# Kernel tuning notes

Measured on AMD Instinct MI355X. Metric: run time of the kernel, lower is better.

Reference implementation:

```python
import jax, jax.numpy as jnp
import numpy as np

BETA = 0.05

def _mogrify(x, h, Qd, Rd):
    x = 2.0 * jax.nn.sigmoid(h @ Qd) * x
    h = 2.0 * jax.nn.sigmoid(x @ Rd) * h
    x = 2.0 * jax.nn.sigmoid(h @ Qd) * x
    h = 2.0 * jax.nn.sigmoid(x @ Rd) * h
    return x, h

def _gru_cell(x, h, Wih, Whh, bih, bhh):
    gi = x @ Wih.T + bih
    gh = h @ Whh.T + bhh
    i_r, i_z, i_n = jnp.split(gi, 3, axis=-1)
    h_r, h_z, h_n = jnp.split(gh, 3, axis=-1)
    r = jax.nn.sigmoid(i_r + h_r)
    z = jax.nn.sigmoid(i_z + h_z)
    n = jnp.tanh(i_n + r * h_n)
    return (1.0 - z) * n + z * h

def _scan_dir(xT, mT, Qd, Rd, Wih, Whh, bih, bhh):
    # xT: [T,B,D], mT: [T,B] bool. Masked GRU scan == packed-sequence semantics.
    B = xT.shape[1]
    H = Whh.shape[1]
    def step(h, inp):
        xt, m = inp
        xm, hm = _mogrify(xt, h, Qd, Rd)
        hn = _gru_cell(xm, hm, Wih, Whh, bih, bhh)
        h = jnp.where(m[:, None], hn, h)
        out = jnp.where(m[:, None], hn, 0.0)
        return h, out
    h0 = jnp.zeros((B, H), xT.dtype)
    _, out = jax.lax.scan(step, h0, (xT, mT))
    return out  # [T,B,H]

def setup_inputs() -> dict:
    key = jax.random.key(0)
    ks = jax.random.split(key, 16)
    B, T, D, H, V, E, S, L = 64, 1024, 256, 256, 50000, 8, 256, 19
    rng = np.random.RandomState(0)
    lens = np.sort(rng.randint(T // 2, T + 1, size=B))[::-1].copy()
    lens[0] = T
    entity_masks = rng.randint(0, 2, size=(B, E)); entity_masks[:, 0] = 1
    slice_masks = rng.randint(0, 2, size=(B, S)); slice_masks[:, 0] = 1
    slice_lens = slice_masks.sum(axis=1).astype(np.float32)
    sc = 1.0 / np.sqrt(H).astype(np.float32)
    inp = {
        'sents': jax.random.randint(ks[0], (B, T), 0, V, dtype=jnp.int32),
        'lens': jnp.asarray(lens, dtype=jnp.int32),
        'entities': jax.random.randint(ks[1], (B, E), 0, T // 2, dtype=jnp.int32),
        'slices': jax.random.randint(ks[2], (B, S), 0, T // 2, dtype=jnp.int32),
        'slice_lens': jnp.asarray(slice_lens),
        'entity_masks': jnp.asarray(entity_masks, dtype=jnp.int32),
        'slice_masks': jnp.asarray(slice_masks, dtype=jnp.int32),
        'emb_table': jax.random.normal(ks[3], (V, D), jnp.float32) * 0.1,
        'Q': jax.random.normal(ks[4], (2, H, D), jnp.float32) * sc,
        'R': jax.random.normal(ks[5], (2, D, H), jnp.float32) * sc,
        'Wih_f': jax.random.normal(ks[6], (3 * H, D), jnp.float32) * sc,
        'Whh_f': jax.random.normal(ks[7], (3 * H, H), jnp.float32) * sc,
        'bih_f': jnp.zeros((3 * H,), jnp.float32),
        'bhh_f': jnp.zeros((3 * H,), jnp.float32),
        'Wih_b': jax.random.normal(ks[8], (3 * H, D), jnp.float32) * sc,
        'Whh_b': jax.random.normal(ks[9], (3 * H, H), jnp.float32) * sc,
        'bih_b': jnp.zeros((3 * H,), jnp.float32),
        'bhh_b': jnp.zeros((3 * H,), jnp.float32),
        'ent_W': jax.random.normal(ks[10], (1, H), jnp.float32) * sc,
        'ent_b': jnp.zeros((1,), jnp.float32),
        'att_w': jax.random.normal(ks[11], (1, H, 1), jnp.float32),
        'dense_W': jax.random.normal(ks[12], (L, H), jnp.float32) * sc,
        'dense_b': jnp.zeros((L,), jnp.float32),
    }
    return inp

def reference(sents, lens, entities, slices, slice_lens, entity_masks, slice_masks,
              emb_table, Q, R, Wih_f, Whh_f, bih_f, bhh_f, Wih_b, Whh_b, bih_b, bhh_b,
              ent_W, ent_b, att_w, dense_W, dense_b):
    B, T = sents.shape
    H = Whh_f.shape[1]
    x = emb_table[sents]                                   # [B,T,D] (dropout = eval identity)
    mask = jnp.arange(T)[None, :] < lens[:, None]          # [B,T]
    xT = jnp.transpose(x, (1, 0, 2))
    mT = mask.T
    out_f = _scan_dir(xT, mT, Q[0], R[0], Wih_f, Whh_f, bih_f, bhh_f)
    out_b = _scan_dir(xT[::-1], mT[::-1], Q[1], R[1], Wih_b, Whh_b, bih_b, bhh_b)[::-1]
    enc = jnp.transpose(out_f + out_b, (1, 0, 2))          # [B,T,H]

    E = entities.shape[1]; S = slices.shape[1]
    ee = jnp.take_along_axis(enc, jnp.broadcast_to(entities[:, :, None].astype(jnp.int32), (B, E, H)), axis=1)
    es = jnp.take_along_axis(enc, jnp.broadcast_to(slices[:, :, None].astype(jnp.int32), (B, S, H)), axis=1)

    # gate_attention
    ew = jnp.squeeze(ee @ ent_W.T + ent_b, axis=-1)        # [B,E]
    ew = jnp.where(entity_masks == 0, -jnp.inf, ew)
    ew = jax.nn.softmax(ew, axis=-1)
    entity = jnp.einsum('be,beh->bh', ew, ee)
    p = jnp.tanh(entity)                                   # [B,H]
    words = jnp.einsum('bsh,bh->bs', es, p)
    words = jnp.where(slice_masks == 0, -jnp.inf, words)
    ww = jax.nn.softmax(words, axis=-1) * slice_lens[:, None]
    rela = jnp.where(ww > BETA, ww, 0.0) / slice_lens[:, None]
    rela = rela / jnp.max(rela, axis=1, keepdims=True)
    Hcat = jnp.concatenate([ee, rela[:, :, None] * es], axis=1)  # [B,E+S,H]

    # attention
    M = jnp.tanh(Hcat)
    a = jnp.einsum('bnh,h->bn', M, att_w[0, :, 0])
    a = jnp.where(a == 0, -jnp.inf, a)
    score = jax.nn.softmax(a, axis=-1)
    att = jnp.einsum('bn,bnh->bh', score, Hcat)
    return jnp.tanh(att) @ dense_W.T + dense_b             # [B,19]
```

## Files before the change

### kernel.cpp

```cpp
#include <hip/hip_runtime.h>
#include <hip/hip_fp16.h>
#include <math.h>

typedef unsigned int uint;

#define Bsz 64
#define Tt  1024
#define TH  512

#define HMF   1280
#define PARTF 1792
#define SMEMF 14080

typedef _Float16 h2 __attribute__((ext_vector_type(2)));
#if defined(__has_builtin)
#if __has_builtin(__builtin_amdgcn_fdot2)
#define HAS_FDOT2 1
#endif
#endif

__device__ __forceinline__ float sigm(float x){ return 1.f/(1.f+expf(-x)); }

#define LG0  asm volatile("s_waitcnt lgkmcnt(0)":::"memory")
#define BAR  __builtin_amdgcn_s_barrier

__device__ __forceinline__ void dot2b(uint w, uint a0, uint a1, float& s0, float& s1){
  h2 wh = __builtin_bit_cast(h2, w);
#ifdef HAS_FDOT2
  s0 = __builtin_amdgcn_fdot2(wh, __builtin_bit_cast(h2,a0), s0, false);
  s1 = __builtin_amdgcn_fdot2(wh, __builtin_bit_cast(h2,a1), s1, false);
#else
  h2 x0 = __builtin_bit_cast(h2,a0), x1 = __builtin_bit_cast(h2,a1);
  s0 = fmaf((float)wh.x,(float)x0.x, fmaf((float)wh.y,(float)x0.y, s0));
  s1 = fmaf((float)wh.x,(float)x1.x, fmaf((float)wh.y,(float)x1.y, s1));
#endif
}

__global__ void pack_k(const float* __restrict__ Q, const float* __restrict__ R,
                       const float* __restrict__ Wih_f, const float* __restrict__ Whh_f,
                       const float* __restrict__ Wih_b, const float* __restrict__ Whh_b,
                       __half* __restrict__ Wh)
{
  int ci = blockIdx.x*256 + threadIdx.x;
  if (ci >= 131072) return;
  float v[8];
  if (ci < 32768){
    bool isR = ci >= 16384;
    int c0 = ci & 16383;
    int c = c0 & 255;
    int rest = c0 >> 8;
    int u = rest & 3, dw = rest >> 2;
    int w = dw & 7, d = dw >> 3;
    const float* S = (isR ? R : Q) + d*65536;
    int k0 = 32*w + 8*u;
    #pragma unroll
    for (int j=0;j<8;++j) v[j] = S[(k0+j)*256 + c];
  } else {
    int c0 = ci - 32768;
    int c = c0 & 255;
    int rest = c0 >> 8;
    int e = rest % 24, dw = rest / 24;
    int w = dw & 7, d = dw >> 3;
    int mat = w & 1, ks = w >> 1;
    int u8 = e / 3, g = e % 3;
    const float* W = mat ? (d? Whh_b : Whh_f) : (d? Wih_b : Wih_f);
    const float* row = W + (size_t)(g*256 + c)*256 + (64*ks + 8*u8);
    #pragma unroll
    for (int j=0;j<8;++j) v[j] = row[j];
  }
  __half h8[8];
  #pragma unroll
  for (int j=0;j<8;++j) h8[j] = __float2half(v[j]);
  *(uint4*)(Wh + (size_t)ci*8) = *(uint4*)h8;
}

__global__ __launch_bounds__(512, 1) void scan_k(
    const int* __restrict__ sents, const int* __restrict__ lens,
    const float* __restrict__ emb,
    const float* __restrict__ bih_f, const float* __restrict__ bhh_f,
    const float* __restrict__ bih_b, const float* __restrict__ bhh_b,
    const __half* __restrict__ Wh, float* __restrict__ enc)
{
  extern __shared__ float sm[];
  __half* smH = (__half*)sm;

  const int bx = blockIdx.x;
  const int dir  = ((bx & 7) >= 4) ? 1 : 0;
  const int pair = (bx >> 3)*4 + (bx & 3);
  const int b0 = pair*2;
  const int tid = threadIdx.x;
  const int wv = tid >> 6, ln = tid & 63;
  const int cj = tid & 255, cb = tid >> 8;
  const int matE = wv & 1, ksE = wv >> 1;

  const __half* QB = Wh + (size_t)((dir*8+wv)*4)*2048;
  const __half* RB = Wh + 131072 + (size_t)((dir*8+wv)*4)*2048;
  const __half* Gp = Wh + 262144 + (size_t)((dir*8+wv)*24)*2048;
  const float* bih = dir ? bih_b : bih_f;
  const float* bhh = dir ? bhh_b : bhh_f;

  const int len0 = lens[b0], len1 = lens[b0+1];
  const int mylen = cb ? len1 : len0;
  const float bi_r = bih[cj], bi_z = bih[cj+256], bi_n = bih[cj+512];
  const float bh_r = bhh[cj], bh_z = bhh[cj+256], bh_n = bhh[cj+512];

  int nsteps, t, tstep;
  if (!dir){ nsteps = TH; t = 0; tstep = 1; }
  else { int mx = max(len0,len1); nsteps = mx; t = mx-1; tstep = -1; }

  smH[512 + tid] = (__half)0.f;

  uint4 Qr[16], Rr[16];
  {
    const uint4* q4 = (const uint4*)QB;
    const uint4* r4 = (const uint4*)RB;
    #pragma unroll
    for (int u=0; u<4; ++u)
      #pragma unroll
      for (int q=0; q<4; ++q){
        Qr[u*4+q] = q4[u*256 + q*64 + ln];
        Rr[u*4+q] = r4[u*256 + q*64 + ln];
      }
  }

  auto dot4 = [&](const uint4& W, const uint4& A0, const uint4& A1, float& a0, float& a1){
    dot2b(W.x, A0.x, A1.x, a0, a1);
    dot2b(W.y, A0.y, A1.y, a0, a1);
    dot2b(W.z, A0.z, A1.z, a0, a1);
    dot2b(W.w, A0.w, A1.w, a0, a1);
  };

  auto mog_part = [&](int actsHO, const uint4 (&W)[16]){
    float2 acc[4];
    acc[0]=acc[1]=acc[2]=acc[3]=make_float2(0.f,0.f);
    #pragma unroll
    for (int u=0; u<4; ++u){
      const int k8 = 4*wv + u;
      const uint4 a0 = *(const uint4*)(smH + actsHO + k8*8);
      const uint4 a1 = *(const uint4*)(smH + actsHO + 256 + k8*8);
      dot4(W[u*4+0], a0, a1, acc[0].x, acc[0].y);
      dot4(W[u*4+1], a0, a1, acc[1].x, acc[1].y);
      dot4(W[u*4+2], a0, a1, acc[2].x, acc[2].y);
      dot4(W[u*4+3], a0, a1, acc[3].x, acc[3].y);
    }
    #pragma unroll
    for (int q=0;q<4;++q)
      *(float2*)(sm + PARTF + wv*512 + (ln+64*q)*2) = acc[q];
  };
  auto mog_fin = [&](float mult, int dstHO, bool alsoF32)->float{
    float ssum = 0.f;
    #pragma unroll
    for (int p=0;p<8;++p) ssum += sm[PARTF + p*512 + cj*2 + cb];
    float val = 2.f*sigm(ssum)*mult;
    smH[dstHO + cb*256 + cj] = (__half)val;
    if (alsoF32) sm[HMF + cb*256 + cj] = val;
    return val;
  };

  uint4 GA[4], GBb[4], GC[4];
  #define LDU(DST, U) do{ const uint4* p_ = (const uint4*)(Gp + (size_t)(U)*2048); \
    DST[0]=p_[ln]; DST[1]=p_[ln+64]; DST[2]=p_[ln+128]; DST[3]=p_[ln+192]; }while(0)
  LDU(GA, 0); LDU(GBb, 1);

  float hprev = 0.f, x1 = 0.f, hm1 = 0.f;
  LG0; BAR();

  for (int s=0; s<nsteps; ++s, t+=tstep){
    int tok = sents[(b0+cb)*Tt + t];
    float x0 = emb[(size_t)tok*256 + cj];

    mog_part(512, Qr);              LG0; BAR();
    x1 = mog_fin(x0, 0, false);     LG0; BAR();
    mog_part(0, Rr);                LG0; BAR();
    hm1 = mog_fin(hprev, 1024, false); LG0; BAR();
    mog_part(1024, Qr);             LG0; BAR();
    x1 = mog_fin(x1, 0, false);     LG0; BAR();
    mog_part(0, Rr);                LG0; BAR();
    mog_fin(hm1, 1024, true);       LG0; BAR();

    {
      const int AFh = matE ? 1024 : 0;
      float2 ag[12];
      #pragma unroll
      for (int i=0;i<12;++i) ag[i] = make_float2(0.f,0.f);

      #define E_STEP(E, CUR, NXT, NU) { \
        LDU(NXT, NU); \
        const int u8_ = (E)/3, g_ = (E) - 3*u8_; \
        const int kb_ = 64*ksE + 8*u8_; \
        const uint4 ea0 = *(const uint4*)(smH + AFh + kb_); \
        const uint4 ea1 = *(const uint4*)(smH + AFh + 256 + kb_); \
        dot4(CUR[0], ea0, ea1, ag[g_*4+0].x, ag[g_*4+0].y); \
        dot4(CUR[1], ea0, ea1, ag[g_*4+1].x, ag[g_*4+1].y); \
        dot4(CUR[2], ea0, ea1, ag[g_*4+2].x, ag[g_*4+2].y); \
        dot4(CUR[3], ea0, ea1, ag[g_*4+3].x, ag[g_*4+3].y); }

      E_STEP(0,  GA,  GC,  2);  E_STEP(1,  GBb, GA,  3);  E_STEP(2,  GC,  GBb, 4);
      E_STEP(3,  GA,  GC,  5);  E_STEP(4,  GBb, GA,  6);  E_STEP(5,  GC,  GBb, 7);
      E_STEP(6,  GA,  GC,  8);  E_STEP(7,  GBb, GA,  9);  E_STEP(8,  GC,  GBb, 10);
      E_STEP(9,  GA,  GC,  11); E_STEP(10, GBb, GA,  12); E_STEP(11, GC,  GBb, 13);
      E_STEP(12, GA,  GC,  14); E_STEP(13, GBb, GA,  15); E_STEP(14, GC,  GBb, 16);
      E_STEP(15, GA,  GC,  17); E_STEP(16, GBb, GA,  18); E_STEP(17, GC,  GBb, 19);
      E_STEP(18, GA,  GC,  20); E_STEP(19, GBb, GA,  21); E_STEP(20, GC,  GBb, 22);
      E_STEP(21, GA,  GC,  23); E_STEP(22, GBb, GA,  0);  E_STEP(23, GC,  GBb, 1);
      #undef E_STEP

      #pragma unroll
      for (int g=0;g<3;++g)
        #pragma unroll
        for (int q=0;q<4;++q)
          *(float2*)(sm + PARTF + wv*1536 + (g*256 + ln + 64*q)*2) = ag[g*4+q];
    }
    LG0; BAR();
    {
      float gi[3], gh[3];
      #pragma unroll
      for (int g=0; g<3; ++g){
        float si = 0.f, sh = 0.f;
        #pragma unroll
        for (int p=0;p<4;++p){
          si += sm[PARTF + (p*2+0)*1536 + (g*256+cj)*2 + cb];
          sh += sm[PARTF + (p*2+1)*1536 + (g*256+cj)*2 + cb];
        }
        gi[g] = si; gh[g] = sh;
      }
      float r = sigm(gi[0]+bi_r + gh[0]+bh_r);
      float z = sigm(gi[1]+bi_z + gh[1]+bh_z);
      float n = tanhf(gi[2]+bi_n + r*(gh[2]+bh_n));
      float hm2v = sm[HMF + cb*256 + cj];
      float uu = (1.f - z)*n + z*hm2v;
      bool m = (t < mylen);
      float hnew = m ? uu : hprev;
      hprev = hnew;
      smH[512 + cb*256 + cj] = (__half)hnew;
      if (m && t < TH)
        atomicAdd(&enc[((size_t)(b0+cb)*TH + t)*256 + cj], uu);
    }
    LG0; BAR();
  }
  #undef LDU
}

__global__ __launch_bounds__(256) void epi_k(
    const float* __restrict__ enc,
    const int* __restrict__ entities, const int* __restrict__ slices,
    const float* __restrict__ slice_lens,
    const int* __restrict__ entity_masks, const int* __restrict__ slice_masks,
    const float* __restrict__ ent_W, const float* __restrict__ ent_b,
    const float* __restrict__ att_w,
    const float* __restrict__ dense_W, const float* __restrict__ dense_b,
    float* __restrict__ out)
{
    const int b = blockIdx.x;
    const int j = threadIdx.x;
    const int wave = j >> 6, lane = j & 63;

    __shared__ float ee[8][256];
    __shared__ float p[256];
    __shared__ float rela[256];
    __shared__ float sc[264];
    __shared__ float red[4];
    __shared__ float aw[256];
    __shared__ int   spos[256];

    aw[j]   = att_w[j];
    spos[j] = slices[b * 256 + j];
    #pragma unroll
    for (int e = 0; e < 8; ++e)
        ee[e][j] = enc[((size_t)b * TH + entities[b * 8 + e]) * 256 + j];
    __syncthreads();

    float entWj = ent_W[j];
    for (int e = 0; e < 8; ++e) {
        float v = ee[e][j] * entWj;
        #pragma unroll
        for (int o = 32; o > 0; o >>= 1) v += __shfl_down(v, o);
        if (lane == 0) red[wave] = v;
        __syncthreads();
        if (j == 0) sc[e] = red[0] + red[1] + red[2] + red[3] + ent_b[0];
        __syncthreads();
    }
    float mx = -INFINITY;
    float ewv[8];
    #pragma unroll
    for (int e = 0; e < 8; ++e) {
        float v = entity_masks[b * 8 + e] ? sc[e] : -INFINITY;
        ewv[e] = v; mx = fmaxf(mx, v);
    }
    float den = 0.f;
    #pragma unroll
    for (int e = 0; e < 8; ++e) {
        ewv[e] = entity_masks[b * 8 + e] ? expf(ewv[e] - mx) : 0.f;
        den += ewv[e];
    }
    float accp = 0.f;
    #pragma unroll
    for (int e = 0; e < 8; ++e) accp += (ewv[e] / den) * ee[e][j];
    p[j] = tanhf(accp);
    __syncthreads();

    for (int s0 = wave; s0 < 256; s0 += 4) {
        const float* row = enc + ((size_t)b * TH + spos[s0]) * 256;
        float v = 0.f;
        #pragma unroll
        for (int i = 0; i < 4; ++i) { int c = lane + 64 * i; v += row[c] * p[c]; }
        #pragma unroll
        for (int o = 32; o > 0; o >>= 1) v += __shfl_down(v, o);
        if (lane == 0) sc[s0] = v;
    }
    __syncthreads();

    float sl  = slice_lens[b];
    int   smk = slice_masks[b * 256 + j];
    float wv  = smk ? sc[j] : -INFINITY;
    float bm = wv;
    #pragma unroll
    for (int o = 32; o > 0; o >>= 1) bm = fmaxf(bm, __shfl_down(bm, o));
    __syncthreads();
    if (lane == 0) red[wave] = bm;
    __syncthreads();
    bm = fmaxf(fmaxf(red[0], red[1]), fmaxf(red[2], red[3]));
    float ex = smk ? expf(wv - bm) : 0.f;
    float sm2 = ex;
    #pragma unroll
    for (int o = 32; o > 0; o >>= 1) sm2 += __shfl_down(sm2, o);
    __syncthreads();
    if (lane == 0) red[wave] = sm2;
    __syncthreads();
    sm2 = red[0] + red[1] + red[2] + red[3];
    float ww = ex / sm2 * sl;
    float rl = (ww > 0.05f) ? (ww / sl) : 0.f;
    float rm = rl;
    #pragma unroll
    for (int o = 32; o > 0; o >>= 1) rm = fmaxf(rm, __shfl_down(rm, o));
    __syncthreads();
    if (lane == 0) red[wave] = rm;
    __syncthreads();
    rm = fmaxf(fmaxf(red[0], red[1]), fmaxf(red[2], red[3]));
    rl = rl / rm;
    rela[j] = rl;
    __syncthreads();

    for (int n = wave; n < 264; n += 4) {
        float v = 0.f;
        if (n < 8) {
            #pragma unroll
            for (int i = 0; i < 4; ++i) { int c = lane + 64 * i; v += tanhf(ee[n][c]) * aw[c]; }
        } else {
            int s0 = n - 8;
            const float* row = enc + ((size_t)b * TH + spos[s0]) * 256;
            float rl2 = rela[s0];
            #pragma unroll
            for (int i = 0; i < 4; ++i) { int c = lane + 64 * i; v += tanhf(rl2 * row[c]) * aw[c]; }
        }
        #pragma unroll
        for (int o = 32; o > 0; o >>= 1) v += __shfl_down(v, o);
        if (lane == 0) sc[n] = v;
    }
    __syncthreads();

    float a1 = sc[j];       a1 = (a1 == 0.f) ? -INFINITY : a1;
    float a2 = (j < 8) ? sc[256 + j] : -INFINITY;
    if (a2 == 0.f) a2 = -INFINITY;
    float am = fmaxf(a1, a2);
    #pragma unroll
    for (int o = 32; o > 0; o >>= 1) am = fmaxf(am, __shfl_down(am, o));
    __syncthreads();
    if (lane == 0) red[wave] = am;
    __syncthreads();
    am = fmaxf(fmaxf(red[0], red[1]), fmaxf(red[2], red[3]));
    float e1 = (a1 == -INFINITY) ? 0.f : expf(a1 - am);
    float e2 = (a2 == -INFINITY) ? 0.f : expf(a2 - am);
    float esum = e1 + e2;
    #pragma unroll
    for (int o = 32; o > 0; o >>= 1) esum += __shfl_down(esum, o);
    __syncthreads();
    if (lane == 0) red[wave] = esum;
    __syncthreads();
    esum = red[0] + red[1] + red[2] + red[3];
    __syncthreads();
    sc[j] = e1 / esum;
    if (j < 8) sc[256 + j] = e2 / esum;
    __syncthreads();

    float att = 0.f;
    #pragma unroll
    for (int n = 0; n < 8; ++n) att += sc[n] * ee[n][j];
    for (int s0 = 0; s0 < 256; ++s0) {
        float scn = sc[8 + s0];
        if (scn > 0.f)
            att += scn * rela[s0] * enc[((size_t)b * TH + spos[s0]) * 256 + j];
    }
    float ta = tanhf(att);

    for (int l = 0; l < 19; ++l) {
        float v = ta * dense_W[l * 256 + j];
        #pragma unroll
        for (int o = 32; o > 0; o >>= 1) v += __shfl_down(v, o);
        __syncthreads();
        if (lane == 0) red[wave] = v;
        __syncthreads();
        if (j == 0) out[b * 19 + l] = red[0] + red[1] + red[2] + red[3] + dense_b[l];
    }
}

extern "C" void kernel_launch(void* const* d_in, const int* in_sizes, int n_in,
                              void* d_out, int out_size, void* d_ws, size_t ws_size,
                              hipStream_t stream) {
    (void)in_sizes; (void)n_in; (void)out_size; (void)ws_size;
    const int*   sents        = (const int*)d_in[0];
    const int*   lens         = (const int*)d_in[1];
    const int*   entities     = (const int*)d_in[2];
    const int*   slices       = (const int*)d_in[3];
    const float* slice_lens   = (const float*)d_in[4];
    const int*   entity_masks = (const int*)d_in[5];
    const int*   slice_masks  = (const int*)d_in[6];
    const float* emb          = (const float*)d_in[7];
    const float* Q            = (const float*)d_in[8];
    const float* R            = (const float*)d_in[9];
    const float* Wih_f        = (const float*)d_in[10];
    const float* Whh_f        = (const float*)d_in[11];
    const float* bih_f        = (const float*)d_in[12];
    const float* bhh_f        = (const float*)d_in[13];
    const float* Wih_b        = (const float*)d_in[14];
    const float* Whh_b        = (const float*)d_in[15];
    const float* bih_b        = (const float*)d_in[16];
    const float* bhh_b        = (const float*)d_in[17];
    const float* ent_W        = (const float*)d_in[18];
    const float* ent_b        = (const float*)d_in[19];
    const float* att_w        = (const float*)d_in[20];
    const float* dense_W      = (const float*)d_in[21];
    const float* dense_b      = (const float*)d_in[22];

    float*  enc = (float*)d_ws;
    __half* Wh  = (__half*)(enc + (size_t)Bsz * TH * 256);

    const int smem_bytes = SMEMF * 4;
    hipFuncSetAttribute(reinterpret_cast<const void*>(scan_k),
                        hipFuncAttributeMaxDynamicSharedMemorySize, smem_bytes);

    hipMemsetAsync(enc, 0, (size_t)Bsz * TH * 256 * sizeof(float), stream);
    pack_k<<<512, 256, 0, stream>>>(Q, R, Wih_f, Whh_f, Wih_b, Whh_b, Wh);
    scan_k<<<64, 512, smem_bytes, stream>>>(sents, lens, emb,
                                            bih_f, bhh_f, bih_b, bhh_b,
                                            Wh, enc);
    epi_k<<<64, 256, 0, stream>>>(enc, entities, slices, slice_lens,
                                  entity_masks, slice_masks, ent_W, ent_b,
                                  att_w, dense_W, dense_b, (float*)d_out);
}
```

Baseline: 11.10 ms.

## Double scan block to 1024 threads and stream mogrifier weights from cache

Each scan block grows from 512 to 1024 threads (16 waves), so every wave handles half as much of the K dimension in the mogrifier and GRU gate matvecs. The Q/R mogrifier weights are no longer held in registers; they are reloaded from global/L2 each sub-step, with a small prefetch of the next matrix slice. Partial sums come from twice as many waves, so shared memory grows and the reductions read more slices, while only the first 512 threads run the elementwise finish steps. The aim is more latency hiding per serial timestep, at the cost of repeated weight traffic, extra reduction work and idle threads during the finish phases.

```diff
diff --git a/kernel.cpp b/kernel.cpp
--- a/kernel.cpp
+++ b/kernel.cpp
@@ -10,7 +10,7 @@
 
 #define HMF   1280
 #define PARTF 1792
-#define SMEMF 14080
+#define SMEMF 26368
 
 typedef _Float16 h2 __attribute__((ext_vector_type(2)));
 #if defined(__has_builtin)
@@ -74,7 +74,7 @@
   *(uint4*)(Wh + (size_t)ci*8) = *(uint4*)h8;
 }
 
-__global__ __launch_bounds__(512, 1) void scan_k(
+__global__ __launch_bounds__(1024) void scan_k(
     const int* __restrict__ sents, const int* __restrict__ lens,
     const float* __restrict__ emb,
     const float* __restrict__ bih_f, const float* __restrict__ bhh_f,
@@ -90,12 +90,19 @@
   const int b0 = pair*2;
   const int tid = threadIdx.x;
   const int wv = tid >> 6, ln = tid & 63;
-  const int cj = tid & 255, cb = tid >> 8;
-  const int matE = wv & 1, ksE = wv >> 1;
-
-  const __half* QB = Wh + (size_t)((dir*8+wv)*4)*2048;
-  const __half* RB = Wh + 131072 + (size_t)((dir*8+wv)*4)*2048;
-  const __half* Gp = Wh + 262144 + (size_t)((dir*8+wv)*24)*2048;
+  const int cj = tid & 255;
+  const int cb = (tid >> 8) & 1;
+  const bool fin = (tid < 512);
+  const int matE = wv & 1, ks8 = wv >> 1;
+
+  const uint4* QB2 = (const uint4*)Wh
+      + (size_t)(((dir*8 + (wv>>1))*4 + (wv&1)*2))*256;
+  const uint4* RB2 = (const uint4*)(Wh + 131072)
+      + (size_t)(((dir*8 + (wv>>1))*4 + (wv&1)*2))*256;
+  const int wold = matE + 2*(ks8>>1);
+  const uint4* Gp4 = (const uint4*)(Wh + 262144)
+      + ((size_t)(dir*8 + wold)*24 + 12*(ks8&1))*256;
+
   const float* bih = dir ? bih_b : bih_f;
   const float* bhh = dir ? bhh_b : bhh_f;
 
@@ -108,20 +115,7 @@
   if (!dir){ nsteps = TH; t = 0; tstep = 1; }
   else { int mx = max(len0,len1); nsteps = mx; t = mx-1; tstep = -1; }
 
-  smH[512 + tid] = (__half)0.f;
-
-  uint4 Qr[16], Rr[16];
-  {
-    const uint4* q4 = (const uint4*)QB;
-    const uint4* r4 = (const uint4*)RB;
-    #pragma unroll
-    for (int u=0; u<4; ++u)
-      #pragma unroll
-      for (int q=0; q<4; ++q){
-        Qr[u*4+q] = q4[u*256 + q*64 + ln];
-        Rr[u*4+q] = r4[u*256 + q*64 + ln];
-      }
-  }
+  if (tid < 512) smH[512 + tid] = (__half)0.f;
 
   auto dot4 = [&](const uint4& W, const uint4& A0, const uint4& A1, float& a0, float& a1){
     dot2b(W.x, A0.x, A1.x, a0, a1);
@@ -130,18 +124,33 @@
     dot2b(W.w, A0.w, A1.w, a0, a1);
   };
 
-  auto mog_part = [&](int actsHO, const uint4 (&W)[16]){
+  uint4 P0, P1, P2, P3;
+  { P0 = QB2[ln]; P1 = QB2[ln+64]; P2 = QB2[ln+128]; P3 = QB2[ln+192]; }
+
+  auto mog_part = [&](int actsHO, const uint4* ub, const uint4* nextb){
+    uint4 W00=P0, W01=P1, W02=P2, W03=P3;
+    uint4 W10 = ub[256+ln], W11 = ub[256+ln+64],
+          W12 = ub[256+ln+128], W13 = ub[256+ln+192];
+    P0 = nextb[ln]; P1 = nextb[ln+64]; P2 = nextb[ln+128]; P3 = nextb[ln+192];
     float2 acc[4];
     acc[0]=acc[1]=acc[2]=acc[3]=make_float2(0.f,0.f);
-    #pragma unroll
-    for (int u=0; u<4; ++u){
-      const int k8 = 4*wv + u;
+    {
+      const int k8 = 2*wv;
       const uint4 a0 = *(const uint4*)(smH + actsHO + k8*8);
       const uint4 a1 = *(const uint4*)(smH + actsHO + 256 + k8*8);
-      dot4(W[u*4+0], a0, a1, acc[0].x, acc[0].y);
-      dot4(W[u*4+1], a0, a1, acc[1].x, acc[1].y);
-      dot4(W[u*4+2], a0, a1, acc[2].x, acc[2].y);
-      dot4(W[u*4+3], a0, a1, acc[3].x, acc[3].y);
+      dot4(W00, a0, a1, acc[0].x, acc[0].y);
+      dot4(W01, a0, a1, acc[1].x, acc[1].y);
+      dot4(W02, a0, a1, acc[2].x, acc[2].y);
+      dot4(W03, a0, a1, acc[3].x, acc[3].y);
+    }
+    {
+      const int k8 = 2*wv + 1;
+      const uint4 a0 = *(const uint4*)(smH + actsHO + k8*8);
+      const uint4 a1 = *(const uint4*)(smH + actsHO + 256 + k8*8);
+      dot4(W10, a0, a1, acc[0].x, acc[0].y);
+      dot4(W11, a0, a1, acc[1].x, acc[1].y);
+      dot4(W12, a0, a1, acc[2].x, acc[2].y);
+      dot4(W13, a0, a1, acc[3].x, acc[3].y);
     }
     #pragma unroll
     for (int q=0;q<4;++q)
@@ -150,7 +159,7 @@
   auto mog_fin = [&](float mult, int dstHO, bool alsoF32)->float{
     float ssum = 0.f;
     #pragma unroll
-    for (int p=0;p<8;++p) ssum += sm[PARTF + p*512 + cj*2 + cb];
+    for (int p=0;p<16;++p) ssum += sm[PARTF + p*512 + cj*2 + cb];
     float val = 2.f*sigm(ssum)*mult;
     smH[dstHO + cb*256 + cj] = (__half)val;
     if (alsoF32) sm[HMF + cb*256 + cj] = val;
@@ -158,36 +167,44 @@
   };
 
   uint4 GA[4], GBb[4], GC[4];
-  #define LDU(DST, U) do{ const uint4* p_ = (const uint4*)(Gp + (size_t)(U)*2048); \
+  #define LDU(DST, U) do{ const uint4* p_ = Gp4 + (size_t)(U)*256; \
     DST[0]=p_[ln]; DST[1]=p_[ln+64]; DST[2]=p_[ln+128]; DST[3]=p_[ln+192]; }while(0)
-  LDU(GA, 0); LDU(GBb, 1);
 
   float hprev = 0.f, x1 = 0.f, hm1 = 0.f;
   LG0; BAR();
 
   for (int s=0; s<nsteps; ++s, t+=tstep){
-    int tok = sents[(b0+cb)*Tt + t];
-    float x0 = emb[(size_t)tok*256 + cj];
-
-    mog_part(512, Qr);              LG0; BAR();
-    x1 = mog_fin(x0, 0, false);     LG0; BAR();
-    mog_part(0, Rr);                LG0; BAR();
-    hm1 = mog_fin(hprev, 1024, false); LG0; BAR();
-    mog_part(1024, Qr);             LG0; BAR();
-    x1 = mog_fin(x1, 0, false);     LG0; BAR();
-    mog_part(0, Rr);                LG0; BAR();
-    mog_fin(hm1, 1024, true);       LG0; BAR();
+    float x0 = 0.f;
+    if (fin){
+      int tok = sents[(b0+cb)*Tt + t];
+      x0 = emb[(size_t)tok*256 + cj];
+    }
+    mog_part(512, QB2, RB2);        LG0; BAR();
+    if (fin) x1 = mog_fin(x0, 0, false);
+    LG0; BAR();
+    mog_part(0, RB2, QB2);          LG0; BAR();
+    if (fin) hm1 = mog_fin(hprev, 1024, false);
+    LG0; BAR();
+    mog_part(1024, QB2, RB2);       LG0; BAR();
+    if (fin) x1 = mog_fin(x1, 0, false);
+    LG0; BAR();
+    mog_part(0, RB2, QB2);
+    LDU(GA, 0); LDU(GBb, 1);
+    LG0; BAR();
+    if (fin) mog_fin(hm1, 1024, true);
+    LG0; BAR();
 
     {
-      const int AFh = matE ? 1024 : 0;
       float2 ag[12];
       #pragma unroll
       for (int i=0;i<12;++i) ag[i] = make_float2(0.f,0.f);
-
-      #define E_STEP(E, CUR, NXT, NU) { \
-        LDU(NXT, NU); \
-        const int u8_ = (E)/3, g_ = (E) - 3*u8_; \
-        const int kb_ = 64*ksE + 8*u8_; \
+      const int AFh = matE ? 1024 : 0;
+      const int kbb = 32*ks8;
+
+      #define E_STEP(E, CUR, NXT, DOLOAD) { \
+        if (DOLOAD) LDU(NXT, (E)+2); \
+        const int g_ = (E) % 3; \
+        const int kb_ = kbb + 8*((E)/3); \
         const uint4 ea0 = *(const uint4*)(smH + AFh + kb_); \
         const uint4 ea1 = *(const uint4*)(smH + AFh + 256 + kb_); \
         dot4(CUR[0], ea0, ea1, ag[g_*4+0].x, ag[g_*4+0].y); \
@@ -195,32 +212,28 @@
         dot4(CUR[2], ea0, ea1, ag[g_*4+2].x, ag[g_*4+2].y); \
         dot4(CUR[3], ea0, ea1, ag[g_*4+3].x, ag[g_*4+3].y); }
 
-      E_STEP(0,  GA,  GC,  2);  E_STEP(1,  GBb, GA,  3);  E_STEP(2,  GC,  GBb, 4);
-      E_STEP(3,  GA,  GC,  5);  E_STEP(4,  GBb, GA,  6);  E_STEP(5,  GC,  GBb, 7);
-      E_STEP(6,  GA,  GC,  8);  E_STEP(7,  GBb, GA,  9);  E_STEP(8,  GC,  GBb, 10);
-      E_STEP(9,  GA,  GC,  11); E_STEP(10, GBb, GA,  12); E_STEP(11, GC,  GBb, 13);
-      E_STEP(12, GA,  GC,  14); E_STEP(13, GBb, GA,  15); E_STEP(14, GC,  GBb, 16);
-      E_STEP(15, GA,  GC,  17); E_STEP(16, GBb, GA,  18); E_STEP(17, GC,  GBb, 19);
-      E_STEP(18, GA,  GC,  20); E_STEP(19, GBb, GA,  21); E_STEP(20, GC,  GBb, 22);
-      E_STEP(21, GA,  GC,  23); E_STEP(22, GBb, GA,  0);  E_STEP(23, GC,  GBb, 1);
+      E_STEP(0,  GA,  GC,  1); E_STEP(1,  GBb, GA,  1); E_STEP(2,  GC,  GBb, 1);
+      E_STEP(3,  GA,  GC,  1); E_STEP(4,  GBb, GA,  1); E_STEP(5,  GC,  GBb, 1);
+      E_STEP(6,  GA,  GC,  1); E_STEP(7,  GBb, GA,  1); E_STEP(8,  GC,  GBb, 1);
+      E_STEP(9,  GA,  GC,  1); E_STEP(10, GBb, GA,  0); E_STEP(11, GC,  GBb, 0);
       #undef E_STEP
 
       #pragma unroll
       for (int g=0;g<3;++g)
         #pragma unroll
         for (int q=0;q<4;++q)
-          *(float2*)(sm + PARTF + wv*1536 + (g*256 + ln + 64*q)*2) = ag[g*4+q];
-    }
-    LG0; BAR();
-    {
+          *(float2*)(sm + PARTF + (ks8*2+matE)*1536 + (g*256 + ln + 64*q)*2) = ag[g*4+q];
+    }
+    LG0; BAR();
+    if (fin){
       float gi[3], gh[3];
       #pragma unroll
       for (int g=0; g<3; ++g){
         float si = 0.f, sh = 0.f;
         #pragma unroll
-        for (int p=0;p<4;++p){
-          si += sm[PARTF + (p*2+0)*1536 + (g*256+cj)*2 + cb];
-          sh += sm[PARTF + (p*2+1)*1536 + (g*256+cj)*2 + cb];
+        for (int k=0;k<8;++k){
+          si += sm[PARTF + (k*2+0)*1536 + (g*256+cj)*2 + cb];
+          sh += sm[PARTF + (k*2+1)*1536 + (g*256+cj)*2 + cb];
         }
         gi[g] = si; gh[g] = sh;
       }
@@ -441,9 +454,9 @@
 
     hipMemsetAsync(enc, 0, (size_t)Bsz * TH * 256 * sizeof(float), stream);
     pack_k<<<512, 256, 0, stream>>>(Q, R, Wih_f, Whh_f, Wih_b, Whh_b, Wh);
-    scan_k<<<64, 512, smem_bytes, stream>>>(sents, lens, emb,
-                                            bih_f, bhh_f, bih_b, bhh_b,
-                                            Wh, enc);
+    scan_k<<<64, 1024, smem_bytes, stream>>>(sents, lens, emb,
+                                             bih_f, bhh_f, bih_b, bhh_b,
+                                             Wh, enc);
     epi_k<<<64, 256, 0, stream>>>(enc, entities, slices, slice_lens,
                                   entity_masks, slice_masks, ent_W, ent_b,
                                   att_w, dense_W, dense_b, (float*)d_out);
```

Measured after the change: 26.60 ms (median of 2 runs). 140% more time.
